# Kernel tuning notes

Measured on AMD Instinct MI355X. Metric: run time of the kernel, lower is better.

## Reference

```python
import jax, jax.numpy as jnp
import numpy as np

N, C, CS, H = 2048, 768, 384, 16
D = C // H  # 48, per-head dim


def _ln(x, eps=1e-5):
    # torch LayerNorm: population variance over last dim
    m = jnp.mean(x, axis=-1, keepdims=True)
    v = jnp.var(x, axis=-1, keepdims=True)
    return (x - m) * jax.lax.rsqrt(v + eps)


def setup_inputs() -> dict:
    key = jax.random.key(0)
    ks = jax.random.split(key, 12)
    s = 0.02  # small init scale for weights
    return {
        "x": jax.random.normal(ks[0], (N, C), jnp.float32),
        "mask": jnp.ones((N,), jnp.float32),
        "pair_logits": jax.random.normal(ks[1], (H, N, N), jnp.float32),
        "single_cond": jax.random.normal(ks[2], (N, CS), jnp.float32),
        "q_w": jax.random.normal(ks[3], (C, C), jnp.float32) * s,
        "q_b": jnp.zeros((C,), jnp.float32),
        "k_w": jax.random.normal(ks[4], (C, C), jnp.float32) * s,
        "v_w": jax.random.normal(ks[5], (C, C), jnp.float32) * s,
        "gate_w": jax.random.normal(ks[6], (C, C), jnp.float32) * s,
        "sc_ln_w": jnp.ones((CS,), jnp.float32),
        "scale_w": jax.random.normal(ks[7], (C, CS), jnp.float32) * s,
        "scale_b": jnp.zeros((C,), jnp.float32),
        "bias_w": jax.random.normal(ks[8], (C, CS), jnp.float32) * s,
        "t2_w": jax.random.normal(ks[9], (C, C), jnp.float32) * s,
        "az_w": jax.random.normal(ks[10], (C, CS), jnp.float32) * s,
        "az_b": jnp.zeros((C,), jnp.float32),
    }


def reference(x, mask, pair_logits, single_cond, q_w, q_b, k_w, v_w, gate_w,
              sc_ln_w, scale_w, scale_b, bias_w, t2_w, az_w, az_b):
    n = x.shape[0]
    mask_bias = (1e9 * (mask - 1.0))[None, None, :]  # (1,1,N) additive bias
    # AdaptiveLayerNorm (use_single_cond=True)
    xn = _ln(x)                                      # no affine
    sc = _ln(single_cond) * sc_ln_w                  # LN with weight, no bias
    xm = jax.nn.sigmoid(sc @ scale_w.T + scale_b) * xn + sc @ bias_w.T
    # qkv projections -> (n, h, d)
    q = (xm @ q_w.T + q_b).reshape(n, H, D)
    k = (xm @ k_w.T).reshape(n, H, D)
    v = (xm @ v_w.T).reshape(n, H, D)
    logits = jnp.einsum('qhc,khc->hqk', q * (D ** -0.5), k) + mask_bias
    logits = logits + pair_logits
    weights = jax.nn.softmax(logits, axis=-1)        # (h, n, n)
    wavg = jnp.einsum('hqk,khc->qhc', weights, v).reshape(n, C)
    wavg = wavg * jax.nn.sigmoid(xm @ gate_w.T)      # sigmoid gating
    # AdaLNZero
    out = wavg @ t2_w.T
    out = jax.nn.sigmoid(single_cond @ az_w.T + az_b) * out
    return out
```

## Files before the change

### kernel.cpp

```cpp
#include <hip/hip_runtime.h>

typedef unsigned short u16;
typedef __attribute__((ext_vector_type(8))) short short8;
typedef __attribute__((ext_vector_type(4))) float f32x4;
typedef __attribute__((ext_vector_type(4))) unsigned short us4;

#define MFMA(a,b,c) __builtin_amdgcn_mfma_f32_16x16x32_bf16(a,b,c,0,0,0)
#define LOG2E 1.44269504088896341f
#define FENCE asm volatile("" ::: "memory")

__device__ __forceinline__ u16 f2bf(float f) {
  unsigned u = __builtin_bit_cast(unsigned, f);
  return (u16)((u + 0x7FFFu + ((u >> 16) & 1u)) >> 16);
}
__device__ __forceinline__ float bf2f(u16 u) {
  return __builtin_bit_cast(float, (unsigned)u << 16);
}
__device__ __forceinline__ unsigned cvtpk(float a, float b) {
  unsigned r;
  asm("v_cvt_pk_bf16_f32 %0, %1, %2" : "=v"(r) : "v"(a), "v"(b));
  return r;
}
__device__ __forceinline__ float sigmoidf_(float x) { return 1.f / (1.f + __expf(-x)); }

__device__ __forceinline__ void gload16(const void* g, void* l) {
  __builtin_amdgcn_global_load_lds(
      (const __attribute__((address_space(1))) void*)g,
      (__attribute__((address_space(3))) void*)l, 16, 0, 0);
}

__global__ __launch_bounds__(256) void cvt_weights(
    const float* __restrict__ sw, const float* __restrict__ bw, const float* __restrict__ aw,
    const float* __restrict__ qw, const float* __restrict__ kw, const float* __restrict__ vw,
    const float* __restrict__ gw, const float* __restrict__ tw,
    u16* __restrict__ wsb, u16* __restrict__ waz, u16* __restrict__ wqkvg, u16* __restrict__ wt2)
{
  long i = ((long)blockIdx.x * 256 + threadIdx.x) * 4;
  const float* src; u16* dst;
  if      (i < 294912)  { src = sw + i;             dst = wsb + i; }
  else if (i < 589824)  { src = bw + (i - 294912);  dst = wsb + i; }
  else if (i < 884736)  { src = aw + (i - 589824);  dst = waz + (i - 589824); }
  else if (i < 1474560) { src = qw + (i - 884736);  dst = wqkvg + (i - 884736); }
  else if (i < 2064384) { src = kw + (i - 1474560); dst = wqkvg + (i - 884736); }
  else if (i < 2654208) { src = vw + (i - 2064384); dst = wqkvg + (i - 884736); }
  else if (i < 3244032) { src = gw + (i - 2654208); dst = wqkvg + (i - 884736); }
  else                  { src = tw + (i - 3244032); dst = wt2 + (i - 3244032); }
  f32x4 v = *(const f32x4*)src;
  us4 o = { f2bf(v[0]), f2bf(v[1]), f2bf(v[2]), f2bf(v[3]) };
  *(us4*)dst = o;
}

__device__ __forceinline__ void blockreduce2(float& a, float& b) {
  #pragma unroll
  for (int d = 1; d < 64; d <<= 1) { a += __shfl_xor(a, d); b += __shfl_xor(b, d); }
  __shared__ float red[8];
  int w = threadIdx.x >> 6, l = threadIdx.x & 63;
  if (l == 0) { red[w] = a; red[4 + w] = b; }
  __syncthreads();
  a = red[0] + red[1] + red[2] + red[3];
  b = red[4] + red[5] + red[6] + red[7];
}

__global__ __launch_bounds__(256) void ln_prep(
    const float* __restrict__ x, const float* __restrict__ sc,
    const float* __restrict__ sc_ln_w, const float* __restrict__ mask,
    float* __restrict__ xn, u16* __restrict__ sc_bf, u16* __restrict__ scr_bf,
    float* __restrict__ mbv)
{
  int bid = blockIdx.x, t = threadIdx.x;
  if (bid < 2048) {
    const float* row = x + (long)bid * 768;
    float v0 = row[t], v1 = row[t + 256], v2 = row[t + 512];
    float s = v0 + v1 + v2, sq = v0*v0 + v1*v1 + v2*v2;
    blockreduce2(s, sq);
    float mean = s * (1.f / 768.f);
    float var = sq * (1.f / 768.f) - mean * mean;
    float rs = rsqrtf(var + 1e-5f);
    float* orow = xn + (long)bid * 768;
    orow[t] = (v0 - mean) * rs; orow[t + 256] = (v1 - mean) * rs; orow[t + 512] = (v2 - mean) * rs;
  } else if (bid < 4096) {
    int r = bid - 2048;
    const float* row = sc + (long)r * 384;
    float v0 = row[t];
    float v1 = (t < 128) ? row[t + 256] : 0.f;
    float s = v0 + v1, sq = v0*v0 + v1*v1;
    blockreduce2(s, sq);
    float mean = s * (1.f / 384.f), var = sq * (1.f / 384.f) - mean * mean;
    float rs = rsqrtf(var + 1e-5f);
    sc_bf[r*384 + t]  = f2bf((v0 - mean) * rs * sc_ln_w[t]);
    scr_bf[r*384 + t] = f2bf(v0);
    if (t < 128) {
      sc_bf[r*384 + t + 256]  = f2bf((v1 - mean) * rs * sc_ln_w[t + 256]);
      scr_bf[r*384 + t + 256] = f2bf(v1);
    }
  } else {
    for (int i = t; i < 2048; i += 256) mbv[i] = 1e9f * (mask[i] - 1.f);
  }
}

__global__ __launch_bounds__(256) void gemm_bf16(
    const u16* __restrict__ X, const u16* __restrict__ W,
    float* __restrict__ Y, int M, int K)
{
  __shared__ u16 lA[4096];
  __shared__ u16 lB[4096];
  const int row0 = blockIdx.x << 7;
  const int col0 = blockIdx.y << 7;
  const int tid = threadIdx.x;
  const int w = tid >> 6, l = tid & 63;
  const int wr = (w >> 1) << 6, wc = (w & 1) << 6;
  const int g = l >> 4, r16 = l & 15;
  const int srow = w * 32 + (l >> 2);
  const int scol = (l & 3) * 8;
  f32x4 acc[4][4] = {};
  for (int k0 = 0; k0 < K; k0 += 32) {
    gload16(X + (long)(row0 + srow) * K + k0 + scol,      &lA[w*1024]);
    gload16(X + (long)(row0 + srow + 16) * K + k0 + scol, &lA[w*1024 + 512]);
    gload16(W + (long)(col0 + srow) * K + k0 + scol,      &lB[w*1024]);
    gload16(W + (long)(col0 + srow + 16) * K + k0 + scol, &lB[w*1024 + 512]);
    __syncthreads();
    short8 af[4], bw_[4];
    #pragma unroll
    for (int i = 0; i < 4; ++i) { af[i]  = *(const short8*)&lA[(wr + i*16 + r16)*32 + g*8]; }
    #pragma unroll
    for (int j = 0; j < 4; ++j) { bw_[j] = *(const short8*)&lB[(wc + j*16 + r16)*32 + g*8]; }
    #pragma unroll
    for (int i = 0; i < 4; ++i) {
      #pragma unroll
      for (int j = 0; j < 4; ++j) {
        acc[i][j] = MFMA(af[i], bw_[j], acc[i][j]);
      }
    }
    __syncthreads();
  }
  #pragma unroll
  for (int i = 0; i < 4; ++i) {
    #pragma unroll
    for (int j = 0; j < 4; ++j) {
      long rr = row0 + wr + i*16 + g*4;
      int cc = col0 + wc + j*16 + r16;
      #pragma unroll
      for (int r = 0; r < 4; ++r) { Y[(rr + r) * M + cc] = acc[i][j][r]; }
    }
  }
}

__global__ __launch_bounds__(256) void gemm_bf16_az(
    const u16* __restrict__ X, const u16* __restrict__ W,
    const float* __restrict__ azs, float* __restrict__ Y, int M, int K)
{
  __shared__ u16 lA[4096];
  __shared__ u16 lB[4096];
  const int row0 = blockIdx.x << 7;
  const int col0 = blockIdx.y << 7;
  const int tid = threadIdx.x;
  const int w = tid >> 6, l = tid & 63;
  const int wr = (w >> 1) << 6, wc = (w & 1) << 6;
  const int g = l >> 4, r16 = l & 15;
  const int srow = w * 32 + (l >> 2);
  const int scol = (l & 3) * 8;
  f32x4 acc[4][4] = {};
  for (int k0 = 0; k0 < K; k0 += 32) {
    gload16(X + (long)(row0 + srow) * K + k0 + scol,      &lA[w*1024]);
    gload16(X + (long)(row0 + srow + 16) * K + k0 + scol, &lA[w*1024 + 512]);
    gload16(W + (long)(col0 + srow) * K + k0 + scol,      &lB[w*1024]);
    gload16(W + (long)(col0 + srow + 16) * K + k0 + scol, &lB[w*1024 + 512]);
    __syncthreads();
    short8 af[4], bw_[4];
    #pragma unroll
    for (int i = 0; i < 4; ++i) { af[i]  = *(const short8*)&lA[(wr + i*16 + r16)*32 + g*8]; }
    #pragma unroll
    for (int j = 0; j < 4; ++j) { bw_[j] = *(const short8*)&lB[(wc + j*16 + r16)*32 + g*8]; }
    #pragma unroll
    for (int i = 0; i < 4; ++i) {
      #pragma unroll
      for (int j = 0; j < 4; ++j) {
        acc[i][j] = MFMA(af[i], bw_[j], acc[i][j]);
      }
    }
    __syncthreads();
  }
  #pragma unroll
  for (int i = 0; i < 4; ++i) {
    #pragma unroll
    for (int j = 0; j < 4; ++j) {
      long rr = row0 + wr + i*16 + g*4;
      int cc = col0 + wc + j*16 + r16;
      #pragma unroll
      for (int r = 0; r < 4; ++r) {
        Y[(rr + r) * M + cc] = acc[i][j][r] * azs[(rr + r) * M + cc];
      }
    }
  }
}

__global__ __launch_bounds__(256) void gemm_qkvg(
    const u16* __restrict__ X, const u16* __restrict__ W,
    const float* __restrict__ q_b,
    u16* __restrict__ qpad, u16* __restrict__ kpad,
    u16* __restrict__ vt, u16* __restrict__ gsig)
{
  __shared__ u16 lA[4096];
  __shared__ u16 lB[4096];
  const int K = 768;
  const int row0 = blockIdx.x << 7;
  const int col0 = blockIdx.y << 7;
  const int tid = threadIdx.x;
  const int w = tid >> 6, l = tid & 63;
  const int wr = (w >> 1) << 6, wc = (w & 1) << 6;
  const int g = l >> 4, r16 = l & 15;
  const int srow = w * 32 + (l >> 2);
  const int scol = (l & 3) * 8;
  f32x4 acc[4][4] = {};
  for (int k0 = 0; k0 < K; k0 += 32) {
    gload16(X + (long)(row0 + srow) * K + k0 + scol,      &lA[w*1024]);
    gload16(X + (long)(row0 + srow + 16) * K + k0 + scol, &lA[w*1024 + 512]);
    gload16(W + (long)(col0 + srow) * K + k0 + scol,      &lB[w*1024]);
    gload16(W + (long)(col0 + srow + 16) * K + k0 + scol, &lB[w*1024 + 512]);
    __syncthreads();
    short8 af[4], bw_[4];
    #pragma unroll
    for (int i = 0; i < 4; ++i) { af[i]  = *(const short8*)&lA[(wr + i*16 + r16)*32 + g*8]; }
    #pragma unroll
    for (int j = 0; j < 4; ++j) { bw_[j] = *(const short8*)&lB[(wc + j*16 + r16)*32 + g*8]; }
    #pragma unroll
    for (int i = 0; i < 4; ++i) {
      #pragma unroll
      for (int j = 0; j < 4; ++j) {
        acc[i][j] = MFMA(af[i], bw_[j], acc[i][j]);
      }
    }
    __syncthreads();
  }
  const int sec = (col0 >= 2304) ? 3 : (col0 >= 1536) ? 2 : (col0 >= 768) ? 1 : 0;
  #pragma unroll
  for (int i = 0; i < 4; ++i) {
    #pragma unroll
    for (int j = 0; j < 4; ++j) {
      int rr = row0 + wr + i*16 + g*4;
      int cc = col0 + wc + j*16 + r16;
      if (sec == 0) {
        int m = cc, h = m / 48, d = m - h * 48;
        float qb = q_b[m];
        #pragma unroll
        for (int r = 0; r < 4; ++r)
          qpad[((long)h*2048 + rr + r)*64 + d] =
              f2bf((acc[i][j][r] + qb) * 0.14433756729740643f);
      } else if (sec == 1) {
        int m = cc - 768, h = m / 48, d = m - h * 48;
        #pragma unroll
        for (int r = 0; r < 4; ++r)
          kpad[((long)h*2048 + rr + r)*64 + d] = f2bf(acc[i][j][r]);
      } else if (sec == 2) {
        int m = cc - 1536, h = m / 48, d = m - h * 48;
        us4 o = { f2bf(acc[i][j][0]), f2bf(acc[i][j][1]),
                  f2bf(acc[i][j][2]), f2bf(acc[i][j][3]) };
        *(us4*)(vt + ((long)h*48 + d)*2048 + rr) = o;
      } else {
        int m = cc - 2304;
        #pragma unroll
        for (int r = 0; r < 4; ++r)
          gsig[(long)(rr + r)*768 + m] = f2bf(sigmoidf_(acc[i][j][r]));
      }
    }
  }
}

__global__ __launch_bounds__(256) void pad_init(
    const float* __restrict__ mbv, u16* __restrict__ qpad, u16* __restrict__ kpad)
{
  int t = blockIdx.x * 256 + threadIdx.x;
  int n = t & 2047;
  long base = (long)t * 64 + 48;
  us4 z = {0, 0, 0, 0};
  us4 q0 = { f2bf(1.0f), 0, 0, 0 };
  us4 k0 = { f2bf(mbv[n]), 0, 0, 0 };
  *(us4*)(qpad + base) = q0;  *(us4*)(qpad + base + 4) = z;
  *(us4*)(qpad + base + 8) = z; *(us4*)(qpad + base + 12) = z;
  *(us4*)(kpad + base) = k0;  *(us4*)(kpad + base + 4) = z;
  *(us4*)(kpad + base + 8) = z; *(us4*)(kpad + base + 12) = z;
}

__global__ __launch_bounds__(256) void ada_kernel(
    const float* __restrict__ Y1, const float* __restrict__ Yaz,
    const float* __restrict__ xn, const float* __restrict__ scale_b,
    const float* __restrict__ az_b, u16* __restrict__ xm, float* __restrict__ azsig)
{
  long e = ((long)blockIdx.x * 256 + threadIdx.x) * 4;
  int n = (int)(e / 768), c = (int)(e % 768);
  f32x4 ys = *(const f32x4*)(Y1 + (long)n*1536 + c);
  f32x4 yb = *(const f32x4*)(Y1 + (long)n*1536 + 768 + c);
  f32x4 xv = *(const f32x4*)(xn + e);
  f32x4 sb = *(const f32x4*)(scale_b + c);
  f32x4 ya = *(const f32x4*)(Yaz + e);
  f32x4 ab = *(const f32x4*)(az_b + c);
  us4 o; f32x4 az;
  #pragma unroll
  for (int k = 0; k < 4; ++k) {
    o[k] = f2bf(sigmoidf_(ys[k] + sb[k]) * xv[k] + yb[k]);
    az[k] = sigmoidf_(ya[k] + ab[k]);
  }
  *(us4*)(xm + e) = o;
  *(f32x4*)(azsig + e) = az;
}

__global__ __launch_bounds__(256, 3) void attn_kernel(
    const u16* __restrict__ qpad, const u16* __restrict__ kpad,
    const u16* __restrict__ vt, const float* __restrict__ pair,
    const u16* __restrict__ gsig, u16* __restrict__ wg)
{
  __shared__ __align__(16) char smem[28672];
  const int bid = blockIdx.x;
  const int h = ((bid & 7) << 1) | ((bid >> 3) & 1);
  const int qb = bid >> 4;
  const int tid = threadIdx.x, w = tid >> 6, l = tid & 63;
  const int g = l >> 4, q = l & 15;
  const int qrow = qb * 64 + w * 16 + q;

  const u16* qbase = qpad + ((long)h * 2048 + qrow) * 64;
  short8 qf0 = *(const short8*)(qbase + g * 8);
  short8 qf1 = *(const short8*)(qbase + 32 + g * 8);

  const float* prow = pair + ((long)h * 2048 + qrow) * 2048;
  const u16*   kgl  = kpad + (long)h * 2048 * 64;
  const u16*   vgl  = vt   + (long)h * 48 * 2048;
  const int sr8 = l >> 3, sc8 = l & 7;

  f32x4 prA[4], prB[4];

  #define STAGE_PR(KT, BUF) do {                                                  \
    _Pragma("unroll")                                                             \
    for (int mf_ = 0; mf_ < 4; ++mf_)                                             \
      BUF[mf_] = __builtin_nontemporal_load(                                      \
          (const f32x4*)(prow + (long)(KT)*64 + mf_*16 + g*4));                   \
  } while (0)

  #define STAGE_KV(KT, BI) do {                                                   \
    char* kd = smem + (BI)*8192 + w*2048;                                          \
    _Pragma("unroll")                                                              \
    for (int i_ = 0; i_ < 2; ++i_) {                                               \
      int row_ = i_*8 + sr8;                                                       \
      gload16(kgl + (long)((KT)*64 + w*16 + row_)*64 + ((sc8 ^ (row_&7)) << 3),    \
              kd + i_*1024);                                                       \
    }                                                                              \
    if (w > 0) {                                                                   \
      char* vd = smem + 16384 + (BI)*6144 + (w-1)*2048;                            \
      _Pragma("unroll")                                                            \
      for (int i_ = 0; i_ < 2; ++i_) {                                             \
        int row_ = i_*8 + sr8;                                                     \
        gload16(vgl + (long)((w-1)*16 + row_)*2048 + (KT)*64 +                     \
                ((sc8 ^ (row_&7)) << 3), vd + i_*1024);                            \
      }                                                                            \
    }                                                                              \
  } while (0)

  STAGE_PR(0, prA); STAGE_KV(0, 0);
  STAGE_PR(1, prB); STAGE_KV(1, 1);

  float m = -1e30f, ssum = 0.f;
  f32x4 o0 = {0,0,0,0}, o1 = {0,0,0,0}, o2 = {0,0,0,0};

  #define BODY(T, PRBUF, PAR) do {                                                \
    if ((T) == 31)   { asm volatile("s_waitcnt vmcnt(0)" ::: "memory"); }          \
    else if (w == 0) { asm volatile("s_waitcnt vmcnt(6)" ::: "memory"); }          \
    else             { asm volatile("s_waitcnt vmcnt(8)" ::: "memory"); }          \
    __builtin_amdgcn_s_barrier();                                                  \
    FENCE;                                                                         \
    const char* kb = smem + (PAR)*8192;                                            \
    const char* vb = smem + 16384 + (PAR)*6144;                                    \
    f32x4 s[4];                                                                    \
    _Pragma("unroll")                                                              \
    for (int mf = 0; mf < 4; ++mf) {                                               \
      const int kr = mf*16 + q;                                                    \
      short8 ka = *(const short8*)(kb + kr*128 + ((g       ^ (q&7)) << 4));        \
      short8 kc = *(const short8*)(kb + kr*128 + (((g + 4) ^ (q&7)) << 4));        \
      s[mf] = MFMA(ka, qf0, PRBUF[mf]);                                            \
      s[mf] = MFMA(kc, qf1, s[mf]);                                                \
    }                                                                              \
    float tmax = -3e38f;                                                           \
    _Pragma("unroll")                                                              \
    for (int mf = 0; mf < 4; ++mf)                                                 \
      tmax = fmaxf(tmax, fmaxf(fmaxf(s[mf][0], s[mf][1]), fmaxf(s[mf][2], s[mf][3])));\
    tmax = fmaxf(tmax, __shfl_xor(tmax, 16));                                      \
    tmax = fmaxf(tmax, __shfl_xor(tmax, 32));                                      \
    float mnew = fmaxf(m, tmax);                                                   \
    float alpha = exp2f((m - mnew) * LOG2E);                                       \
    m = mnew;                                                                      \
    float mL = mnew * LOG2E;                                                       \
    float psum = 0.f;                                                              \
    unsigned pk0[4], pk1[4];                                                       \
    _Pragma("unroll")                                                              \
    for (int mf = 0; mf < 4; ++mf) {                                               \
      float p0 = exp2f(fmaf(s[mf][0], LOG2E, -mL));                                \
      float p1 = exp2f(fmaf(s[mf][1], LOG2E, -mL));                                \
      float p2 = exp2f(fmaf(s[mf][2], LOG2E, -mL));                                \
      float p3 = exp2f(fmaf(s[mf][3], LOG2E, -mL));                                \
      psum += (p0 + p1) + (p2 + p3);                                               \
      pk0[mf] = cvtpk(p0, p1);                                                     \
      pk1[mf] = cvtpk(p2, p3);                                                     \
    }                                                                              \
    ssum = ssum * alpha + psum;                                                    \
    o0 *= alpha; o1 *= alpha; o2 *= alpha;                                         \
    const int laneA = ((g & 1) << 5) + q;                                          \
    const int laneB = laneA + 16;                                                  \
    const bool hi = g >= 2;                                                        \
    _Pragma("unroll")                                                              \
    for (int ks = 0; ks < 2; ++ks) {                                               \
      unsigned w0a = __shfl(pk0[2*ks], laneA), w0b = __shfl(pk0[2*ks+1], laneA);   \
      unsigned w1a = __shfl(pk1[2*ks], laneA), w1b = __shfl(pk1[2*ks+1], laneA);   \
      unsigned w2a = __shfl(pk0[2*ks], laneB), w2b = __shfl(pk0[2*ks+1], laneB);   \
      unsigned w3a = __shfl(pk1[2*ks], laneB), w3b = __shfl(pk1[2*ks+1], laneB);   \
      union { unsigned u[4]; short8 v; } pf;                                       \
      pf.u[0] = hi ? w0b : w0a;                                                    \
      pf.u[1] = hi ? w1b : w1a;                                                    \
      pf.u[2] = hi ? w2b : w2a;                                                    \
      pf.u[3] = hi ? w3b : w3a;                                                    \
      const int vc = ((ks*4 + g) ^ (q & 7)) << 4;                                  \
      short8 v0 = *(const short8*)(vb + (q)*128      + vc);                        \
      short8 v1 = *(const short8*)(vb + (16 + q)*128 + vc);                        \
      short8 v2 = *(const short8*)(vb + (32 + q)*128 + vc);                        \
      o0 = MFMA(v0, pf.v, o0);                                                     \
      o1 = MFMA(v1, pf.v, o1);                                                     \
      o2 = MFMA(v2, pf.v, o2);                                                     \
    }                                                                              \
    FENCE;                                                                         \
    __builtin_amdgcn_s_barrier();                                                  \
    FENCE;                                                                         \
    if ((T) < 30) { STAGE_PR((T)+2, PRBUF); STAGE_KV((T)+2, PAR); }                \
    __builtin_amdgcn_sched_barrier(0);                                             \
  } while (0)

  for (int t = 0; t < 32; t += 2) {
    BODY(t,     prA, 0);
    BODY(t + 1, prB, 1);
  }
  #undef BODY
  #undef STAGE_PR
  #undef STAGE_KV

  ssum += __shfl_xor(ssum, 16);
  ssum += __shfl_xor(ssum, 32);
  float rinv = 1.f / ssum;
  const long nbase = (long)qrow * 768 + h * 48;
  #pragma unroll
  for (int r = 0; r < 3; ++r) {
    f32x4 ov = (r == 0) ? o0 : ((r == 1) ? o1 : o2);
    int c = r * 16 + g * 4;
    us4 gs = *(const us4*)(gsig + nbase + c);
    us4 ou;
    #pragma unroll
    for (int j = 0; j < 4; ++j) ou[j] = f2bf(ov[j] * rinv * bf2f(gs[j]));
    *(us4*)(wg + nbase + c) = ou;
  }
}

extern "C" void kernel_launch(void* const* d_in, const int* in_sizes, int n_in,
                              void* d_out, int out_size, void* d_ws, size_t ws_size,
                              hipStream_t stream) {
  const float* x       = (const float*)d_in[0];
  const float* mask    = (const float*)d_in[1];
  const float* pair    = (const float*)d_in[2];
  const float* sc      = (const float*)d_in[3];
  const float* q_w     = (const float*)d_in[4];
  const float* q_b     = (const float*)d_in[5];
  const float* k_w     = (const float*)d_in[6];
  const float* v_w     = (const float*)d_in[7];
  const float* g_w     = (const float*)d_in[8];
  const float* slw     = (const float*)d_in[9];
  const float* scale_w = (const float*)d_in[10];
  const float* scale_b = (const float*)d_in[11];
  const float* bias_w  = (const float*)d_in[12];
  const float* t2_w    = (const float*)d_in[13];
  const float* az_w    = (const float*)d_in[14];
  const float* az_b    = (const float*)d_in[15];
  float* out = (float*)d_out;
  char* ws = (char*)d_ws;

  u16*   Wsb   = (u16*)  (ws + 0);
  u16*   Waz   = (u16*)  (ws + 1179648);
  u16*   Wqkvg = (u16*)  (ws + 1769472);
  u16*   Wt2   = (u16*)  (ws + 6488064);
  float* xn    = (float*)(ws + 7667712);
  u16*   sc_bf = (u16*)  (ws + 13959168);
  u16*   scr_bf= (u16*)  (ws + 15532032);
  u16*   wg    = (u16*)  (ws + 13959168);
  float* mb    = (float*)(ws + 17104896);
  float* Y1    = (float*)(ws + 17113088);
  u16*   qpad  = (u16*)  (ws + 17113088);
  u16*   kpad  = (u16*)  (ws + 21307392);
  float* Yaz   = (float*)(ws + 29696000);
  u16*   xm    = (u16*)  (ws + 35987456);
  float* azsig = (float*)(ws + 39133184);
  u16*   vt    = (u16*)  (ws + 70590464);
  u16*   gsig  = (u16*)  (ws + 73736192);

  cvt_weights<<<3744, 256, 0, stream>>>(scale_w, bias_w, az_w, q_w, k_w, v_w, g_w, t2_w,
                                        Wsb, Waz, Wqkvg, Wt2);
  ln_prep<<<4097, 256, 0, stream>>>(x, sc, slw, mask, xn, sc_bf, scr_bf, mb);
  gemm_bf16<<<dim3(16, 12), 256, 0, stream>>>(sc_bf, Wsb, Y1, 1536, 384);
  gemm_bf16<<<dim3(16, 6), 256, 0, stream>>>(scr_bf, Waz, Yaz, 768, 384);
  ada_kernel<<<1536, 256, 0, stream>>>(Y1, Yaz, xn, scale_b, az_b, xm, azsig);
  gemm_qkvg<<<dim3(16, 24), 256, 0, stream>>>(xm, Wqkvg, q_b, qpad, kpad, vt, gsig);
  pad_init<<<128, 256, 0, stream>>>(mb, qpad, kpad);
  attn_kernel<<<512, 256, 0, stream>>>(qpad, kpad, vt, pair, gsig, wg);
  gemm_bf16_az<<<dim3(16, 6), 256, 0, stream>>>(wg, Wt2, azsig, out, 768, 768);
}
```

Baseline: 187.2 us.

## Shrink small GEMM tiles to 64x64 and route attention P through LDS

The three small GEMMs (scale/bias, az and the final output projection) now use 64x64 tiles instead of 128x128, launching four times as many blocks so more CUs are busy on these small problem sizes. In the attention kernel, the bf16 probability fragments are no longer redistributed with cross-lane shuffles. Each wave writes them to a swizzled per-wave LDS region and reads them back as MFMA B operands. This adds 8 KB of LDS per block, which may reduce occupancy, and lowers data reuse per block in the GEMMs.

```diff
diff --git a/kernel.cpp b/kernel.cpp
--- a/kernel.cpp
+++ b/kernel.cpp
@@ -98,45 +98,41 @@
   }
 }
 
-__global__ __launch_bounds__(256) void gemm_bf16(
+__global__ __launch_bounds__(256) void gemm_bf16_64(
     const u16* __restrict__ X, const u16* __restrict__ W,
     float* __restrict__ Y, int M, int K)
 {
-  __shared__ u16 lA[4096];
-  __shared__ u16 lB[4096];
-  const int row0 = blockIdx.x << 7;
-  const int col0 = blockIdx.y << 7;
+  __shared__ u16 lA[2048];
+  __shared__ u16 lB[2048];
+  const int row0 = blockIdx.x << 6;
+  const int col0 = blockIdx.y << 6;
   const int tid = threadIdx.x;
   const int w = tid >> 6, l = tid & 63;
-  const int wr = (w >> 1) << 6, wc = (w & 1) << 6;
+  const int wr = (w >> 1) << 5, wc = (w & 1) << 5;
   const int g = l >> 4, r16 = l & 15;
-  const int srow = w * 32 + (l >> 2);
+  const int srow = w * 16 + (l >> 2);
   const int scol = (l & 3) * 8;
-  f32x4 acc[4][4] = {};
+  f32x4 acc[2][2] = {};
   for (int k0 = 0; k0 < K; k0 += 32) {
-    gload16(X + (long)(row0 + srow) * K + k0 + scol,      &lA[w*1024]);
-    gload16(X + (long)(row0 + srow + 16) * K + k0 + scol, &lA[w*1024 + 512]);
-    gload16(W + (long)(col0 + srow) * K + k0 + scol,      &lB[w*1024]);
-    gload16(W + (long)(col0 + srow + 16) * K + k0 + scol, &lB[w*1024 + 512]);
-    __syncthreads();
-    short8 af[4], bw_[4];
-    #pragma unroll
-    for (int i = 0; i < 4; ++i) { af[i]  = *(const short8*)&lA[(wr + i*16 + r16)*32 + g*8]; }
-    #pragma unroll
-    for (int j = 0; j < 4; ++j) { bw_[j] = *(const short8*)&lB[(wc + j*16 + r16)*32 + g*8]; }
-    #pragma unroll
-    for (int i = 0; i < 4; ++i) {
+    gload16(X + (long)(row0 + srow) * K + k0 + scol, &lA[w*512]);
+    gload16(W + (long)(col0 + srow) * K + k0 + scol, &lB[w*512]);
+    __syncthreads();
+    short8 af[2], bw_[2];
+    #pragma unroll
+    for (int i = 0; i < 2; ++i) { af[i]  = *(const short8*)&lA[(wr + i*16 + r16)*32 + g*8]; }
+    #pragma unroll
+    for (int j = 0; j < 2; ++j) { bw_[j] = *(const short8*)&lB[(wc + j*16 + r16)*32 + g*8]; }
+    #pragma unroll
+    for (int i = 0; i < 2; ++i)
       #pragma unroll
-      for (int j = 0; j < 4; ++j) {
+      for (int j = 0; j < 2; ++j)
         acc[i][j] = MFMA(af[i], bw_[j], acc[i][j]);
-      }
-    }
-    __syncthreads();
-  }
-  #pragma unroll
-  for (int i = 0; i < 4; ++i) {
-    #pragma unroll
-    for (int j = 0; j < 4; ++j) {
+    __syncthreads();
+  }
+  #pragma unroll
+  for (int i = 0; i < 2; ++i) {
+    #pragma unroll
+    for (int j = 0; j < 2; ++j) {
       long rr = row0 + wr + i*16 + g*4;
       int cc = col0 + wc + j*16 + r16;
       #pragma unroll
@@ -145,45 +141,41 @@
   }
 }
 
-__global__ __launch_bounds__(256) void gemm_bf16_az(
+__global__ __launch_bounds__(256) void gemm_az64(
     const u16* __restrict__ X, const u16* __restrict__ W,
     const float* __restrict__ azs, float* __restrict__ Y, int M, int K)
 {
-  __shared__ u16 lA[4096];
-  __shared__ u16 lB[4096];
-  const int row0 = blockIdx.x << 7;
-  const int col0 = blockIdx.y << 7;
+  __shared__ u16 lA[2048];
+  __shared__ u16 lB[2048];
+  const int row0 = blockIdx.x << 6;
+  const int col0 = blockIdx.y << 6;
   const int tid = threadIdx.x;
   const int w = tid >> 6, l = tid & 63;
-  const int wr = (w >> 1) << 6, wc = (w & 1) << 6;
+  const int wr = (w >> 1) << 5, wc = (w & 1) << 5;
   const int g = l >> 4, r16 = l & 15;
-  const int srow = w * 32 + (l >> 2);
+  const int srow = w * 16 + (l >> 2);
   const int scol = (l & 3) * 8;
-  f32x4 acc[4][4] = {};
+  f32x4 acc[2][2] = {};
   for (int k0 = 0; k0 < K; k0 += 32) {
-    gload16(X + (long)(row0 + srow) * K + k0 + scol,      &lA[w*1024]);
-    gload16(X + (long)(row0 + srow + 16) * K + k0 + scol, &lA[w*1024 + 512]);
-    gload16(W + (long)(col0 + srow) * K + k0 + scol,      &lB[w*1024]);
-    gload16(W + (long)(col0 + srow + 16) * K + k0 + scol, &lB[w*1024 + 512]);
-    __syncthreads();
-    short8 af[4], bw_[4];
-    #pragma unroll
-    for (int i = 0; i < 4; ++i) { af[i]  = *(const short8*)&lA[(wr + i*16 + r16)*32 + g*8]; }
-    #pragma unroll
-    for (int j = 0; j < 4; ++j) { bw_[j] = *(const short8*)&lB[(wc + j*16 + r16)*32 + g*8]; }
-    #pragma unroll
-    for (int i = 0; i < 4; ++i) {
+    gload16(X + (long)(row0 + srow) * K + k0 + scol, &lA[w*512]);
+    gload16(W + (long)(col0 + srow) * K + k0 + scol, &lB[w*512]);
+    __syncthreads();
+    short8 af[2], bw_[2];
+    #pragma unroll
+    for (int i = 0; i < 2; ++i) { af[i]  = *(const short8*)&lA[(wr + i*16 + r16)*32 + g*8]; }
+    #pragma unroll
+    for (int j = 0; j < 2; ++j) { bw_[j] = *(const short8*)&lB[(wc + j*16 + r16)*32 + g*8]; }
+    #pragma unroll
+    for (int i = 0; i < 2; ++i)
       #pragma unroll
-      for (int j = 0; j < 4; ++j) {
+      for (int j = 0; j < 2; ++j)
         acc[i][j] = MFMA(af[i], bw_[j], acc[i][j]);
-      }
-    }
-    __syncthreads();
-  }
-  #pragma unroll
-  for (int i = 0; i < 4; ++i) {
-    #pragma unroll
-    for (int j = 0; j < 4; ++j) {
+    __syncthreads();
+  }
+  #pragma unroll
+  for (int i = 0; i < 2; ++i) {
+    #pragma unroll
+    for (int j = 0; j < 2; ++j) {
       long rr = row0 + wr + i*16 + g*4;
       int cc = col0 + wc + j*16 + r16;
       #pragma unroll
@@ -309,7 +301,7 @@
     const u16* __restrict__ vt, const float* __restrict__ pair,
     const u16* __restrict__ gsig, u16* __restrict__ wg)
 {
-  __shared__ __align__(16) char smem[28672];
+  __shared__ __align__(16) char smem[36864];
   const int bid = blockIdx.x;
   const int h = ((bid & 7) << 1) | ((bid >> 3) & 1);
   const int qb = bid >> 4;
@@ -325,6 +317,8 @@
   const u16*   kgl  = kpad + (long)h * 2048 * 64;
   const u16*   vgl  = vt   + (long)h * 48 * 2048;
   const int sr8 = l >> 3, sc8 = l & 7;
+  unsigned* pl = (unsigned*)(smem + 28672) + w*512 + q*32;
+  const int sx = (q & 7) << 2;
 
   f32x4 prA[4], prB[4];
 
@@ -401,20 +395,18 @@
     }                                                                              \
     ssum = ssum * alpha + psum;                                                    \
     o0 *= alpha; o1 *= alpha; o2 *= alpha;                                         \
-    const int laneA = ((g & 1) << 5) + q;                                          \
-    const int laneB = laneA + 16;                                                  \
-    const bool hi = g >= 2;                                                        \
+               \
+    _Pragma("unroll")                                                              \
+    for (int mf = 0; mf < 4; ++mf) {                                               \
+      uint2 pv_; pv_.x = pk0[mf]; pv_.y = pk1[mf];                                 \
+      *(uint2*)(pl + ((mf*8 + g*2) ^ sx)) = pv_;                                   \
+    }                                                                              \
+    asm volatile("s_waitcnt lgkmcnt(0)" ::: "memory");                             \
+    __builtin_amdgcn_sched_barrier(0);                                             \
     _Pragma("unroll")                                                              \
     for (int ks = 0; ks < 2; ++ks) {                                               \
-      unsigned w0a = __shfl(pk0[2*ks], laneA), w0b = __shfl(pk0[2*ks+1], laneA);   \
-      unsigned w1a = __shfl(pk1[2*ks], laneA), w1b = __shfl(pk1[2*ks+1], laneA);   \
-      unsigned w2a = __shfl(pk0[2*ks], laneB), w2b = __shfl(pk0[2*ks+1], laneB);   \
-      unsigned w3a = __shfl(pk1[2*ks], laneB), w3b = __shfl(pk1[2*ks+1], laneB);   \
-      union { unsigned u[4]; short8 v; } pf;                                       \
-      pf.u[0] = hi ? w0b : w0a;                                                    \
-      pf.u[1] = hi ? w1b : w1a;                                                    \
-      pf.u[2] = hi ? w2b : w2a;                                                    \
-      pf.u[3] = hi ? w3b : w3a;                                                    \
+      union { uint4 u4; short8 v; } pf;                                            \
+      pf.u4 = *(const uint4*)(pl + ((ks*16 + g*4) ^ sx));                          \
       const int vc = ((ks*4 + g) ^ (q & 7)) << 4;                                  \
       short8 v0 = *(const short8*)(vb + (q)*128      + vc);                        \
       short8 v1 = *(const short8*)(vb + (16 + q)*128 + vc);                        \
@@ -497,11 +489,11 @@
   cvt_weights<<<3744, 256, 0, stream>>>(scale_w, bias_w, az_w, q_w, k_w, v_w, g_w, t2_w,
                                         Wsb, Waz, Wqkvg, Wt2);
   ln_prep<<<4097, 256, 0, stream>>>(x, sc, slw, mask, xn, sc_bf, scr_bf, mb);
-  gemm_bf16<<<dim3(16, 12), 256, 0, stream>>>(sc_bf, Wsb, Y1, 1536, 384);
-  gemm_bf16<<<dim3(16, 6), 256, 0, stream>>>(scr_bf, Waz, Yaz, 768, 384);
+  gemm_bf16_64<<<dim3(32, 24), 256, 0, stream>>>(sc_bf, Wsb, Y1, 1536, 384);
+  gemm_bf16_64<<<dim3(32, 12), 256, 0, stream>>>(scr_bf, Waz, Yaz, 768, 384);
   ada_kernel<<<1536, 256, 0, stream>>>(Y1, Yaz, xn, scale_b, az_b, xm, azsig);
   gemm_qkvg<<<dim3(16, 24), 256, 0, stream>>>(xm, Wqkvg, q_b, qpad, kpad, vt, gsig);
   pad_init<<<128, 256, 0, stream>>>(mb, qpad, kpad);
   attn_kernel<<<512, 256, 0, stream>>>(qpad, kpad, vt, pair, gsig, wg);
-  gemm_bf16_az<<<dim3(16, 6), 256, 0, stream>>>(wg, Wt2, azsig, out, 768, 768);
-}
+  gemm_az64<<<dim3(32, 12), 256, 0, stream>>>(wg, Wt2, azsig, out, 768, 768);
+}
```

Result: faster. 167.1 us (-10.7%).
